# Kernel optimization log

Measured on AMD Instinct MI355X. Metric: run time of the kernel, lower is better.

The kernel has to match this reference:

```python
import jax, jax.numpy as jnp
from jax import lax
import numpy as np

DIM = 8
C = 192
N = 198  # 2 special tokens + 14*14 patches (distilled=True)
B = 1024


def quick_gelu(x):
    return x * jax.nn.sigmoid(1.702 * x)


def setup_inputs() -> dict:
    key = jax.random.key(0)
    ks = jax.random.split(key, 7)
    return {
        "x": jax.random.normal(ks[0], (B, N, C), dtype=jnp.float32),
        "w_down": jax.random.normal(ks[1], (DIM, C), dtype=jnp.float32) * 0.05,
        "b_down": jnp.zeros((DIM,), dtype=jnp.float32),
        "conv_w": jax.random.normal(ks[2], (DIM, DIM, 3, 3), dtype=jnp.float32) * 0.05,
        "conv_b": jnp.zeros((DIM,), dtype=jnp.float32),
        "w_up": jax.random.normal(ks[3], (C, DIM), dtype=jnp.float32) * 0.05,
        "b_up": jnp.zeros((C,), dtype=jnp.float32),
    }


def _conv3x3(t, conv_w, conv_b):
    # t: [B, dim, H, W]; 3x3, stride 1, pad 1 (SAME)
    y = lax.conv_general_dilated(
        t, conv_w, window_strides=(1, 1), padding=((1, 1), (1, 1)),
        dimension_numbers=("NCHW", "OIHW", "NCHW"))
    return y + conv_b[None, :, None, None]


def reference(x, w_down, b_down, conv_w, conv_b, w_up, b_up):
    b, n, c = x.shape
    dim = w_down.shape[0]
    # down projection + QuickGELU
    d = quick_gelu(jnp.einsum("bnc,dc->bnd", x, w_down) + b_down)
    # patch tokens -> [B, dim, 14, 14] -> conv -> [B, 196, dim]
    x_patch = d[:, 2:].reshape(b, 14, 14, dim).transpose(0, 3, 1, 2)
    x_patch = _conv3x3(x_patch, conv_w, conv_b)
    x_patch = x_patch.transpose(0, 2, 3, 1).reshape(b, 14 * 14, dim)
    # cls token -> [B, dim, 1, 1] -> conv (only center tap contributes) -> [B, 1, dim]
    x_cls = d[:, :1].reshape(b, 1, 1, dim).transpose(0, 3, 1, 2)
    x_cls = _conv3x3(x_cls, conv_w, conv_b)
    x_cls = x_cls.transpose(0, 2, 3, 1).reshape(b, 1, dim)
    zero_dist = jnp.zeros_like(x_cls)
    d2 = jnp.concatenate([x_cls, zero_dist, x_patch], axis=1)
    d2 = quick_gelu(d2)  # dropout is identity in eval mode
    return jnp.einsum("bnd,cd->bnc", d2, w_up) + b_up
```

## Files before the change

### kernel.cpp

```cpp
#include <hip/hip_runtime.h>
#include <math.h>

#define NTOK 198
#define CCH  192

typedef float vf4 __attribute__((ext_vector_type(4)));

__device__ __forceinline__ float qgelu(float v) {
    return v / (1.0f + __expf(-1.702f * v));
}

__device__ __forceinline__ float dot8(const float4& a, const float4& wa,
                                      const float4& b, const float4& wb) {
    return a.x*wa.x + a.y*wa.y + a.z*wa.z + a.w*wa.w
         + b.x*wb.x + b.y*wb.y + b.z*wb.z + b.w*wb.w;
}

__global__ __launch_bounds__(256, 4) void convpass_fused(
    const float* __restrict__ x,
    const float* __restrict__ w_down,
    const float* __restrict__ b_down,
    const float* __restrict__ conv_w,
    const float* __restrict__ conv_b,
    const float* __restrict__ w_up,
    const float* __restrict__ b_up,
    float* __restrict__ out)
{
    const int half = blockIdx.x;
    const int b    = blockIdx.y;
    const int tid  = threadIdx.x;

    const int d_start   = half ? 86  : 0;
    const int d_count   = half ? 112 : 114;
    const int out_start = half ? 100 : 0;
    const int out_count = half ? 98  : 100;

    __shared__ float s_d[114 * 8];
    __shared__ float s_d2[100 * 8];
    __shared__ float s_cw[576];
    __shared__ float s_cb[8];

    for (int t = tid; t < 576; t += 256) {
        const int kk = t >> 6, rem = t & 63, o = rem >> 3, i = rem & 7;
        s_cw[t] = conv_w[(o * 8 + i) * 9 + kk];
    }
    if (tid < 8) s_cb[tid] = conv_b[tid];

    {
        const int lane  = tid & 63;
        const int wv    = tid >> 6;
        const int chunk = lane >> 3;
        const int dim   = lane & 7;

        float wreg[24];
        {
            const float* wp = w_down + dim * CCH + chunk * 24;
            #pragma unroll
            for (int j = 0; j < 24; ++j) wreg[j] = wp[j];
        }
        const float bd  = b_down[dim];
        const float* xb = x + (size_t)b * NTOK * CCH + chunk * 24;

        #pragma unroll 1
        for (int i = 0; i < 29; ++i) {
            const int idx = i * 4 + wv;
            const bool valid = (idx < d_count);
            const int n = d_start + (valid ? idx : 0);
            const float* xr = xb + (size_t)n * CCH;
            float a0 = 0.f, a1 = 0.f;
            #pragma unroll
            for (int j = 0; j < 3; ++j) {
                const float4 xv = *(const float4*)(xr + j * 8);
                const float4 xw = *(const float4*)(xr + j * 8 + 4);
                a0 += xv.x*wreg[j*8]   + xv.y*wreg[j*8+1] + xv.z*wreg[j*8+2] + xv.w*wreg[j*8+3];
                a1 += xw.x*wreg[j*8+4] + xw.y*wreg[j*8+5] + xw.z*wreg[j*8+6] + xw.w*wreg[j*8+7];
            }
            float acc = a0 + a1;
            acc += __shfl_xor(acc, 8);
            acc += __shfl_xor(acc, 16);
            acc += __shfl_xor(acc, 32);
            if (valid && lane < 8) s_d[idx * 8 + dim] = qgelu(acc + bd);
        }
    }
    __syncthreads();

    for (int j = tid; j < out_count * 8; j += 256) {
        const int nr = j >> 3, o = j & 7;
        const int n = out_start + nr;
        if (n == 1) {
            s_d2[j] = 0.0f;
        } else if (n == 0) {
            const float4 d0 = *(const float4*)&s_d[0];
            const float4 d1 = *(const float4*)&s_d[4];
            const float4 w0 = *(const float4*)&s_cw[4 * 64 + o * 8];
            const float4 w1 = *(const float4*)&s_cw[4 * 64 + o * 8 + 4];
            s_d2[j] = qgelu(s_cb[o] + dot8(d0, w0, d1, w1));
        } else {
            const int pos = n - 2, h = pos / 14, w = pos % 14;
            float acc = s_cb[o];
            #pragma unroll
            for (int dh = -1; dh <= 1; ++dh) {
                const int hh = h + dh;
                if (hh < 0 || hh > 13) continue;
                #pragma unroll
                for (int dw = -1; dw <= 1; ++dw) {
                    const int ww = w + dw;
                    if (ww < 0 || ww > 13) continue;
                    const int tok = 2 + hh * 14 + ww;
                    const int kk  = (dh + 1) * 3 + (dw + 1);
                    const int ti  = tok - d_start;
                    const float4 d0 = *(const float4*)&s_d[ti * 8];
                    const float4 d1 = *(const float4*)&s_d[ti * 8 + 4];
                    const float4 w0 = *(const float4*)&s_cw[kk * 64 + o * 8];
                    const float4 w1 = *(const float4*)&s_cw[kk * 64 + o * 8 + 4];
                    acc += dot8(d0, w0, d1, w1);
                }
            }
            s_d2[j] = qgelu(acc);
        }
    }
    __syncthreads();

    const int c4 = tid % 48;
    const int tl = tid / 48;
    if (tl < 5) {
        float w_r[4][8];
        #pragma unroll
        for (int cc = 0; cc < 4; ++cc) {
            const float4 wa = *(const float4*)(w_up + (c4 * 4 + cc) * 8);
            const float4 wb = *(const float4*)(w_up + (c4 * 4 + cc) * 8 + 4);
            w_r[cc][0] = wa.x; w_r[cc][1] = wa.y; w_r[cc][2] = wa.z; w_r[cc][3] = wa.w;
            w_r[cc][4] = wb.x; w_r[cc][5] = wb.y; w_r[cc][6] = wb.z; w_r[cc][7] = wb.w;
        }
        const float4 bu = *(const float4*)(b_up + c4 * 4);
        float* outb = out + ((size_t)b * NTOK + out_start) * CCH;
        #pragma unroll 1
        for (int nr = tl; nr < out_count; nr += 5) {
            const float4 da = *(const float4*)&s_d2[nr * 8];
            const float4 dv = *(const float4*)&s_d2[nr * 8 + 4];
            float accs[4] = {bu.x, bu.y, bu.z, bu.w};
            #pragma unroll
            for (int cc = 0; cc < 4; ++cc) {
                accs[cc] += da.x * w_r[cc][0] + da.y * w_r[cc][1]
                          + da.z * w_r[cc][2] + da.w * w_r[cc][3]
                          + dv.x * w_r[cc][4] + dv.y * w_r[cc][5]
                          + dv.z * w_r[cc][6] + dv.w * w_r[cc][7];
            }
            const vf4 r = {accs[0], accs[1], accs[2], accs[3]};
            __builtin_nontemporal_store(r, (vf4*)(outb + (size_t)nr * CCH + c4 * 4));
        }
    }
}

extern "C" void kernel_launch(void* const* d_in, const int* in_sizes, int n_in,
                              void* d_out, int out_size, void* d_ws, size_t ws_size,
                              hipStream_t stream) {
    const float* x      = (const float*)d_in[0];
    const float* w_down = (const float*)d_in[1];
    const float* b_down = (const float*)d_in[2];
    const float* conv_w = (const float*)d_in[3];
    const float* conv_b = (const float*)d_in[4];
    const float* w_up   = (const float*)d_in[5];
    const float* b_up   = (const float*)d_in[6];
    float* out = (float*)d_out;

    const int B = in_sizes[0] / (NTOK * CCH);
    convpass_fused<<<dim3(2, B), dim3(256), 0, stream>>>(
        x, w_down, b_down, conv_w, conv_b, w_up, b_up, out);
}
```

Baseline: 77.67 us.

## Process one full batch item per 512-thread block instead of two halves

Replaces the two-block-per-sample split, which recomputed 28 overlapping halo tokens, with a single 512-thread block per sample covering all 198 tokens. This drops the redundant down-projection of halo tokens and halves the number of blocks. In exchange, each block is larger and uses more shared memory, and the 512-thread launch bound may limit registers per thread and occupancy.

```diff
diff --git a/kernel.cpp b/kernel.cpp
--- a/kernel.cpp
+++ b/kernel.cpp
@@ -16,7 +16,7 @@
          + b.x*wb.x + b.y*wb.y + b.z*wb.z + b.w*wb.w;
 }
 
-__global__ __launch_bounds__(256, 4) void convpass_fused(
+__global__ __launch_bounds__(512, 4) void convpass_fused(
     const float* __restrict__ x,
     const float* __restrict__ w_down,
     const float* __restrict__ b_down,
@@ -26,21 +26,15 @@
     const float* __restrict__ b_up,
     float* __restrict__ out)
 {
-    const int half = blockIdx.x;
-    const int b    = blockIdx.y;
-    const int tid  = threadIdx.x;
+    const int b   = blockIdx.x;
+    const int tid = threadIdx.x;
 
-    const int d_start   = half ? 86  : 0;
-    const int d_count   = half ? 112 : 114;
-    const int out_start = half ? 100 : 0;
-    const int out_count = half ? 98  : 100;
-
-    __shared__ float s_d[114 * 8];
-    __shared__ float s_d2[100 * 8];
+    __shared__ float s_d[NTOK * 8];
+    __shared__ float s_d2[NTOK * 8];
     __shared__ float s_cw[576];
     __shared__ float s_cb[8];
 
-    for (int t = tid; t < 576; t += 256) {
+    for (int t = tid; t < 576; t += 512) {
         const int kk = t >> 6, rem = t & 63, o = rem >> 3, i = rem & 7;
         s_cw[t] = conv_w[(o * 8 + i) * 9 + kk];
     }
@@ -62,10 +56,10 @@
         const float* xb = x + (size_t)b * NTOK * CCH + chunk * 24;
 
         #pragma unroll 1
-        for (int i = 0; i < 29; ++i) {
-            const int idx = i * 4 + wv;
-            const bool valid = (idx < d_count);
-            const int n = d_start + (valid ? idx : 0);
+        for (int i = 0; i < 25; ++i) {
+            const int idx = i * 8 + wv;
+            const bool valid = (idx < NTOK);
+            const int n = valid ? idx : 0;
             const float* xr = xb + (size_t)n * CCH;
             float a0 = 0.f, a1 = 0.f;
             #pragma unroll
@@ -84,9 +78,8 @@
     }
     __syncthreads();
 
-    for (int j = tid; j < out_count * 8; j += 256) {
-        const int nr = j >> 3, o = j & 7;
-        const int n = out_start + nr;
+    for (int j = tid; j < NTOK * 8; j += 512) {
+        const int n = j >> 3, o = j & 7;
         if (n == 1) {
             s_d2[j] = 0.0f;
         } else if (n == 0) {
@@ -108,9 +101,8 @@
                     if (ww < 0 || ww > 13) continue;
                     const int tok = 2 + hh * 14 + ww;
                     const int kk  = (dh + 1) * 3 + (dw + 1);
-                    const int ti  = tok - d_start;
-                    const float4 d0 = *(const float4*)&s_d[ti * 8];
-                    const float4 d1 = *(const float4*)&s_d[ti * 8 + 4];
+                    const float4 d0 = *(const float4*)&s_d[tok * 8];
+                    const float4 d1 = *(const float4*)&s_d[tok * 8 + 4];
                     const float4 w0 = *(const float4*)&s_cw[kk * 64 + o * 8];
                     const float4 w1 = *(const float4*)&s_cw[kk * 64 + o * 8 + 4];
                     acc += dot8(d0, w0, d1, w1);
@@ -123,7 +115,7 @@
 
     const int c4 = tid % 48;
     const int tl = tid / 48;
-    if (tl < 5) {
+    if (tl < 10) {
         float w_r[4][8];
         #pragma unroll
         for (int cc = 0; cc < 4; ++cc) {
@@ -133,9 +125,9 @@
             w_r[cc][4] = wb.x; w_r[cc][5] = wb.y; w_r[cc][6] = wb.z; w_r[cc][7] = wb.w;
         }
         const float4 bu = *(const float4*)(b_up + c4 * 4);
-        float* outb = out + ((size_t)b * NTOK + out_start) * CCH;
+        float* outb = out + (size_t)b * NTOK * CCH;
         #pragma unroll 1
-        for (int nr = tl; nr < out_count; nr += 5) {
+        for (int nr = tl; nr < NTOK; nr += 10) {
             const float4 da = *(const float4*)&s_d2[nr * 8];
             const float4 dv = *(const float4*)&s_d2[nr * 8 + 4];
             float accs[4] = {bu.x, bu.y, bu.z, bu.w};
@@ -165,6 +157,6 @@
     float* out = (float*)d_out;
 
     const int B = in_sizes[0] / (NTOK * CCH);
-    convpass_fused<<<dim3(2, B), dim3(256), 0, stream>>>(
+    convpass_fused<<<dim3(B), dim3(512), 0, stream>>>(
         x, w_down, b_down, conv_w, conv_b, w_up, b_up, out);
 }
```

After: 76.96 us. No clear change (-0.9%).
